# Optimization experiments

Measured on AMD Instinct MI355X. Metric: run time of the kernel, lower is better.

The kernel has to match this reference:

```python
import jax, jax.numpy as jnp
import numpy as np

B, C, H, W = 8, 1024, 32, 32   # batch, in_channels (cnn==vit), spatial
OUT = 2048                     # out_channels
NHEAD = 32                     # heads -> head_dim 64
EMBED_DIM = 1024               # used ONLY for the softmax scale (faithful to source)
LN_EPS = 1e-5


def setup_inputs() -> dict:
    key = jax.random.key(0)
    ks = jax.random.split(key, 8)
    f = lambda k, s: jax.random.normal(k, s, dtype=jnp.float32)
    return {
        "x_cnn": f(ks[0], (B, C, H, W)),
        "x_vit": f(ks[1], (B, C, H, W)),
        "Wq": f(ks[2], (OUT, C)) * 0.02, "bq": jnp.zeros((OUT,), jnp.float32),
        "Wk": f(ks[3], (OUT, C)) * 0.02, "bk": jnp.zeros((OUT,), jnp.float32),
        "Wv": f(ks[4], (OUT, C)) * 0.02, "bv": jnp.zeros((OUT,), jnp.float32),
        "w_mix": jnp.float32(0.5),
        "ln_g": jnp.ones((OUT,), jnp.float32), "ln_b": jnp.zeros((OUT,), jnp.float32),
        "Wfc": f(ks[5], (OUT, OUT)) * 0.02, "bfc": jnp.zeros((OUT,), jnp.float32),
    }


def _mha(Q, K, V):
    # Q,K,V: [b, n, OUT] -> multi-head attention, scale by sqrt(EMBED_DIM) as in source
    b, n, _ = Q.shape
    d = OUT // NHEAD
    Qh = Q.reshape(b, n, NHEAD, d)
    Kh = K.reshape(b, n, NHEAD, d)
    Vh = V.reshape(b, n, NHEAD, d)
    scores = jnp.einsum('bqhd,bkhd->bhqk', Qh, Kh) / jnp.sqrt(jnp.float32(EMBED_DIM))
    attn = jax.nn.softmax(scores, axis=-1)
    out = jnp.einsum('bhqk,bkhd->bqhd', attn, Vh)
    return out.reshape(b, n, OUT)


def reference(x_cnn, x_vit, Wq, bq, Wk, bk, Wv, bv, w_mix, ln_g, ln_b, Wfc, bfc):
    b, c, h, w = x_cnn.shape
    xc = x_cnn.reshape(b, c, h * w).transpose(0, 2, 1)   # [b, hw, c]
    xv = x_vit.reshape(b, c, h * w).transpose(0, 2, 1)
    # shared projections, two cross directions
    Q1 = xc @ Wq.T + bq; K1 = xv @ Wk.T + bk; V1 = xv @ Wv.T + bv
    Q2 = xv @ Wq.T + bq; K2 = xc @ Wk.T + bk; V2 = xc @ Wv.T + bv
    attended_vit = _mha(Q1, K1, V1)   # cnn queries attend vit
    attended_cnn = _mha(Q2, K2, V2)   # vit queries attend cnn
    r = attended_cnn * w_mix + attended_vit * (1.0 - w_mix)
    # LayerNorm over last dim (population variance, like torch)
    mu = jnp.mean(r, axis=-1, keepdims=True)
    var = jnp.var(r, axis=-1, keepdims=True)
    r = (r - mu) / jnp.sqrt(var + LN_EPS) * ln_g + ln_b
    r = r @ Wfc.T + bfc
    return r.transpose(0, 2, 1).reshape(b, OUT, h, w)
```

## Files before the change

### kernel.cpp

```cpp
#include <hip/hip_runtime.h>
#include <stdint.h>

typedef unsigned short u16;
typedef unsigned int u32;
typedef __attribute__((ext_vector_type(4))) float float4v;
typedef __attribute__((ext_vector_type(4))) unsigned int uint4v;
typedef __attribute__((ext_vector_type(4))) unsigned short u16x4;
typedef __attribute__((ext_vector_type(8))) short s16x8;
typedef __attribute__((ext_vector_type(4))) float f32x4;

__device__ __forceinline__ float bf2f(u16 h) {
    union { u32 u; float f; } v; v.u = ((u32)h) << 16; return v.f;
}
__device__ __forceinline__ u16 f2bf(float f) {
    union { float f; u32 u; } v; v.f = f;
    return (u16)((v.u + 0x8000u) >> 16);
}
__device__ __forceinline__ float exp2_fast(float x) {
    float r; asm("v_exp_f32 %0, %1" : "=v"(r) : "v"(x)); return r;
}

__device__ __forceinline__ bool detect_f32(const u16* lng) {
    return *(const u32*)lng == 0x3F800000u;
}

__device__ __forceinline__ float read_wmix(const void* wmix) {
    u32 word = *(const u32*)wmix;
    if ((word & 0xFFFFu) == 0u) {
        union { u32 u; float f; } v; v.u = word; return v.f;
    }
    return bf2f((u16)(word & 0xFFFFu));
}

__device__ __forceinline__ uint4v load8(const void* base, long long off, bool isF32) {
    if (isF32) {
        const float* p = (const float*)base + off;
        float4v f0 = *(const float4v*)p;
        float4v f1 = *(const float4v*)(p + 4);
        uint4v r; u16* h = (u16*)&r;
#pragma unroll
        for (int i = 0; i < 4; ++i) { h[i] = f2bf(f0[i]); h[4 + i] = f2bf(f1[i]); }
        return r;
    }
    return *(const uint4v*)((const u16*)base + off);
}
__device__ __forceinline__ float loadraw(const void* p, int idx, bool isF32) {
    return isF32 ? ((const float*)p)[idx] : bf2f(((const u16*)p)[idx]);
}

__global__ __launch_bounds__(256) void convert_w(
    const void* __restrict__ src, u16* __restrict__ dst, int n,
    const u16* __restrict__ lng)
{
    bool f32 = detect_f32(lng);
    long long i = ((long long)blockIdx.x * 256 + threadIdx.x) * 8;
    if (i >= n) return;
    uint4v v = load8(src, i, f32);
    *(uint4v*)(dst + i) = v;
}

__global__ __launch_bounds__(256) void transpose_k(
    const void* __restrict__ xc, const void* __restrict__ xv,
    u16* __restrict__ xt, const u16* __restrict__ lng)
{
    bool f32 = detect_f32(lng);
    int z = blockIdx.z;
    const void* xbase = (z < 8 ? xc : xv);
    long long soff = (long long)(z & 7) * 1024 * 1024;
    u16* outp = xt + (long long)z * 1024 * 1024;
    int c0 = blockIdx.x * 64, p0 = blockIdx.y * 64;
    __shared__ u16 t[64][72];
    int tid = threadIdx.x;
    int cl = tid >> 3, ch = tid & 7;
#pragma unroll
    for (int pass = 0; pass < 2; ++pass) {
        int c = cl + pass * 32;
        uint4v v = load8(xbase, soff + (long long)(c0 + c) * 1024 + p0 + ch * 8, f32);
        const u16* vv = (const u16*)&v;
#pragma unroll
        for (int i = 0; i < 8; ++i) t[ch * 8 + i][c] = vv[i];
    }
    __syncthreads();
#pragma unroll
    for (int pass = 0; pass < 2; ++pass) {
        int p = cl + pass * 32;
        uint4v v; u16* vv = (u16*)&v;
#pragma unroll
        for (int i = 0; i < 8; ++i) vv[i] = t[p][ch * 8 + i];
        *(uint4v*)(outp + (long long)(p0 + p) * 1024 + c0 + ch * 8) = v;
    }
}

__global__ __launch_bounds__(256) void transpose_v(
    const u16* __restrict__ V, u16* __restrict__ VT)
{
    int b = blockIdx.z, head = blockIdx.y, p0 = blockIdx.x * 64;
    const u16* src = V + (long long)b * 1024 * 2048 + head * 64;
    u16* dst = VT + (long long)(b * 32 + head) * 64 * 1024;
    __shared__ u16 t[64][72];
    int tid = threadIdx.x;
    int r = tid >> 3, ch = tid & 7;
#pragma unroll
    for (int pass = 0; pass < 2; ++pass) {
        int p = r + pass * 32;
        uint4v v = *(const uint4v*)(src + (long long)(p0 + p) * 2048 + ch * 8);
        const u16* vv = (const u16*)&v;
#pragma unroll
        for (int i = 0; i < 8; ++i) t[ch * 8 + i][p] = vv[i];
    }
    __syncthreads();
#pragma unroll
    for (int pass = 0; pass < 2; ++pass) {
        int d = r + pass * 32;
        uint4v v = *(const uint4v*)&t[d][ch * 8];
        *(uint4v*)(dst + (long long)d * 1024 + p0 + ch * 8) = v;
    }
}

__global__ __launch_bounds__(256) void gemm_mfma(
    const void* __restrict__ A, int lda, long long sA, int a_raw,
    const void* __restrict__ B, int ldb, long long sB, int b_raw,
    const void* __restrict__ bias,
    void* __restrict__ Cv, int ldc, long long sC, int c_f32,
    int K, int bias_on_m, const u16* __restrict__ lng)
{
    bool f32 = detect_f32(lng);
    bool aF = f32 && a_raw, bF = f32 && b_raw;
    int gx = gridDim.x, gy = gridDim.y, gz = gridDim.z;
    int flat = blockIdx.x + gx * (blockIdx.y + gy * blockIdx.z);
    int nwg = gx * gy * gz;
    int wsw = ((nwg & 7) == 0) ? ((flat & 7) * (nwg >> 3) + (flat >> 3)) : flat;
    int bxi = wsw % gx, rem = wsw / gx;
    int byi = rem % gy, z = rem / gy;

    long long aoff = (long long)z * sA, boff = (long long)z * sB;
    long long coff = (long long)z * sC;
    int m0 = bxi * 128, n0 = byi * 128;
    int tid = threadIdx.x;
    int lane = tid & 63, wave = tid >> 6;
    int lrow = lane & 15, lgrp = lane >> 4;
    int wm = (wave >> 1) * 64, wn = (wave & 1) * 64;

    __shared__ u16 As[128][72];
    __shared__ u16 Bs[128][72];

    f32x4 acc[4][4];
#pragma unroll
    for (int i = 0; i < 4; ++i)
#pragma unroll
        for (int j = 0; j < 4; ++j) acc[i][j] = (f32x4)0.f;

    int sr = tid >> 3;
    int kc = (tid & 7) * 8;

    long long arow[4], brow[4];
#pragma unroll
    for (int q = 0; q < 4; ++q) {
        arow[q] = aoff + (long long)(m0 + sr + q * 32) * lda;
        brow[q] = boff + (long long)(n0 + sr + q * 32) * ldb;
    }

    uint4v an[4], bn[4];
#pragma unroll
    for (int q = 0; q < 4; ++q) {
        an[q] = load8(A, arow[q] + kc, aF);
        bn[q] = load8(B, brow[q] + kc, bF);
    }

    for (int k0 = 0; k0 < K; k0 += 64) {
        uint4v ac[4], bc[4];
#pragma unroll
        for (int q = 0; q < 4; ++q) { ac[q] = an[q]; bc[q] = bn[q]; }
        __syncthreads();
#pragma unroll
        for (int q = 0; q < 4; ++q) {
            *(uint4v*)&As[sr + q * 32][kc] = ac[q];
            *(uint4v*)&Bs[sr + q * 32][kc] = bc[q];
        }
        __syncthreads();
        if (k0 + 64 < K) {
#pragma unroll
            for (int q = 0; q < 4; ++q) {
                an[q] = load8(A, arow[q] + k0 + 64 + kc, aF);
                bn[q] = load8(B, brow[q] + k0 + 64 + kc, bF);
            }
        }
#pragma unroll
        for (int kk = 0; kk < 2; ++kk) {
            s16x8 af[4], bfr[4];
#pragma unroll
            for (int i = 0; i < 4; ++i)
                af[i] = *(const s16x8*)&As[wm + i * 16 + lrow][kk * 32 + lgrp * 8];
#pragma unroll
            for (int j = 0; j < 4; ++j)
                bfr[j] = *(const s16x8*)&Bs[wn + j * 16 + lrow][kk * 32 + lgrp * 8];
#pragma unroll
            for (int i = 0; i < 4; ++i)
#pragma unroll
                for (int j = 0; j < 4; ++j)
                    acc[i][j] = __builtin_amdgcn_mfma_f32_16x16x32_bf16(
                        af[i], bfr[j], acc[i][j], 0, 0, 0);
        }
    }

    float bnj[4];
#pragma unroll
    for (int j = 0; j < 4; ++j)
        bnj[j] = bias_on_m ? 0.f : loadraw(bias, n0 + wn + j * 16 + lrow, f32);
#pragma unroll
    for (int i = 0; i < 4; ++i) {
#pragma unroll
        for (int e = 0; e < 4; ++e) {
            int mrow = m0 + wm + i * 16 + lgrp * 4 + e;
            float bm = bias_on_m ? loadraw(bias, mrow, f32) : 0.f;
#pragma unroll
            for (int j = 0; j < 4; ++j) {
                int ncol = n0 + wn + j * 16 + lrow;
                float val = acc[i][j][e] + (bias_on_m ? bm : bnj[j]);
                long long idx = coff + (long long)mrow * ldc + ncol;
                if (c_f32) ((float*)Cv)[idx] = val;
                else       ((u16*)Cv)[idx] = f2bf(val);
            }
        }
    }
}

__global__ __launch_bounds__(256) void attn_mfma(
    u16* __restrict__ Qb, const u16* __restrict__ Kb, const u16* __restrict__ VTb)
{
    const int ld = 2048;
    const float SCL = 0.0450985123f;
    int flat = blockIdx.x + 16 * (blockIdx.y + 32 * blockIdx.z);
    int w = (flat & 7) * 512 + (flat >> 3);
    int qt = w & 15, head = (w >> 4) & 31, bz = w >> 9;
    int q0 = qt * 64;
    long long base = (long long)bz * 1024 * ld + head * 64;
    u16* Q = Qb + base;
    const u16* K = Kb + base;
    const u16* VT = VTb + (long long)(bz * 32 + head) * 64 * 1024;

    int tid = threadIdx.x;
    int wave = tid >> 6, lane = tid & 63;
    int lrow = lane & 15, lgrp = lane >> 4;

    __shared__ u16 Kt[64][72];
    __shared__ u16 VTt[64][72];
    __shared__ u16 Pt[4][16][72];

    int qw = q0 + wave * 16;
    s16x8 qf0, qf1;
    {
        const u16* qp = Q + (long long)(qw + lrow) * ld + lgrp * 8;
        qf0 = *(const s16x8*)qp;
        qf1 = *(const s16x8*)(qp + 32);
    }

    f32x4 of[4];
#pragma unroll
    for (int dt = 0; dt < 4; ++dt) of[dt] = (f32x4)0.f;
    float mL = 0.f, l_run = 0.f;

    int skey = tid >> 2, sc4 = tid & 3;
    const u16* kptr = K + (long long)skey * ld + sc4 * 8;
    const u16* vptr = VT + (long long)skey * 1024 + sc4 * 16;
    uint4v ka0 = *(const uint4v*)kptr;
    uint4v ka1 = *(const uint4v*)(kptr + 32);
    uint4v va0 = *(const uint4v*)vptr;
    uint4v va1 = *(const uint4v*)(vptr + 8);

    for (int t = 0; t < 16; ++t) {
        *(uint4v*)&Kt[skey][sc4 * 8]       = ka0;
        *(uint4v*)&Kt[skey][sc4 * 8 + 32]  = ka1;
        *(uint4v*)&VTt[skey][sc4 * 16]     = va0;
        *(uint4v*)&VTt[skey][sc4 * 16 + 8] = va1;
        if (t < 15) {
            kptr += 64 * ld;
            vptr += 64;
            ka0 = *(const uint4v*)kptr;
            ka1 = *(const uint4v*)(kptr + 32);
            va0 = *(const uint4v*)vptr;
            va1 = *(const uint4v*)(vptr + 8);
        }
        __syncthreads();

        f32x4 sf[4];
#pragma unroll
        for (int f = 0; f < 4; ++f) {
            s16x8 kf0 = *(const s16x8*)&Kt[f * 16 + lrow][lgrp * 8];
            s16x8 kf1 = *(const s16x8*)&Kt[f * 16 + lrow][lgrp * 8 + 32];
            f32x4 a = (f32x4)0.f;
            a = __builtin_amdgcn_mfma_f32_16x16x32_bf16(kf0, qf0, a, 0, 0, 0);
            a = __builtin_amdgcn_mfma_f32_16x16x32_bf16(kf1, qf1, a, 0, 0, 0);
            sf[f] = a;
        }

        float mx = sf[0][0];
#pragma unroll
        for (int f = 0; f < 4; ++f)
#pragma unroll
            for (int i = 0; i < 4; ++i) mx = fmaxf(mx, sf[f][i]);
        mx = fmaxf(mx, __shfl_xor(mx, 16));
        mx = fmaxf(mx, __shfl_xor(mx, 32));
        if (__any(mx * SCL > mL + 8.f)) {
            float mLn = fmaxf(mL, mx * SCL);
            float sc = exp2_fast(mL - mLn);
            l_run *= sc;
#pragma unroll
            for (int dt = 0; dt < 4; ++dt)
#pragma unroll
                for (int i = 0; i < 4; ++i) of[dt][i] *= sc;
            mL = mLn;
        }

        float nmL = -mL, rs = 0.f;
#pragma unroll
        for (int f = 0; f < 4; ++f) {
            u16x4 pk;
#pragma unroll
            for (int i = 0; i < 4; ++i) {
                float pe = exp2_fast(fmaf(sf[f][i], SCL, nmL));
                rs += pe;
                pk[i] = f2bf(pe);
            }
            *(u16x4*)&Pt[wave][lrow][f * 16 + lgrp * 4] = pk;
        }
        rs += __shfl_xor(rs, 16);
        rs += __shfl_xor(rs, 32);
        l_run += rs;
        asm volatile("s_waitcnt lgkmcnt(0)" ::: "memory");
        __builtin_amdgcn_sched_barrier(0);

#pragma unroll
        for (int kk = 0; kk < 2; ++kk) {
            s16x8 pb = *(const s16x8*)&Pt[wave][lrow][kk * 32 + lgrp * 8];
#pragma unroll
            for (int dt = 0; dt < 4; ++dt) {
                s16x8 va = *(const s16x8*)&VTt[dt * 16 + lrow][kk * 32 + lgrp * 8];
                of[dt] = __builtin_amdgcn_mfma_f32_16x16x32_bf16(va, pb, of[dt], 0, 0, 0);
            }
        }
        __syncthreads();
    }

    float linv = 1.f / l_run;
#pragma unroll
    for (int dt = 0; dt < 4; ++dt) {
        u16x4 o;
#pragma unroll
        for (int i = 0; i < 4; ++i) o[i] = f2bf(of[dt][i] * linv);
        *(u16x4*)(Q + (long long)(qw + lrow) * ld + dt * 16 + lgrp * 4) = o;
    }
}

__global__ __launch_bounds__(256) void mix_ln_k(
    const u16* __restrict__ Avit, const u16* __restrict__ Acnn,
    const void* __restrict__ wmix,
    const void* __restrict__ g, const void* __restrict__ bta,
    u16* __restrict__ Y, const u16* __restrict__ lng)
{
    bool f32 = detect_f32(lng);
    long long row = blockIdx.x;
    const u16* a0 = Avit + row * 2048;
    const u16* a1 = Acnn + row * 2048;
    int tid = threadIdx.x, lane = tid & 63, wave = tid >> 6;
    float w = read_wmix(wmix);
    int o = tid * 8;
    uint4v x0 = *(const uint4v*)(a0 + o);
    uint4v x1 = *(const uint4v*)(a1 + o);
    const u16* p0 = (const u16*)&x0;
    const u16* p1 = (const u16*)&x1;
    float r[8], sum = 0.f, sq = 0.f;
#pragma unroll
    for (int e = 0; e < 8; ++e) {
        r[e] = w * bf2f(p1[e]) + (1.f - w) * bf2f(p0[e]);
        sum += r[e]; sq += r[e] * r[e];
    }
#pragma unroll
    for (int off = 1; off < 64; off <<= 1) {
        sum += __shfl_xor(sum, off);
        sq += __shfl_xor(sq, off);
    }
    __shared__ float red[8];
    if (lane == 0) { red[wave] = sum; red[4 + wave] = sq; }
    __syncthreads();
    sum = red[0] + red[1] + red[2] + red[3];
    sq = red[4] + red[5] + red[6] + red[7];
    float mu = sum * (1.f / 2048.f);
    float var = sq * (1.f / 2048.f) - mu * mu;
    float rstd = rsqrtf(var + 1e-5f);
    uint4v y; u16* py = (u16*)&y;
#pragma unroll
    for (int e = 0; e < 8; ++e)
        py[e] = f2bf((r[e] - mu) * rstd * loadraw(g, o + e, f32) + loadraw(bta, o + e, f32));
    *(uint4v*)(Y + row * 2048 + o) = y;
}

extern "C" void kernel_launch(void* const* d_in, const int* in_sizes, int n_in,
                              void* d_out, int out_size, void* d_ws, size_t ws_size,
                              hipStream_t stream)
{
    const void* x_cnn = d_in[0];
    const void* x_vit = d_in[1];
    const void* Wq = d_in[2];
    const void* bq = d_in[3];
    const void* Wk = d_in[4];
    const void* bk = d_in[5];
    const void* Wv = d_in[6];
    const void* bv = d_in[7];
    const void* wmix = d_in[8];
    const u16* ln_g = (const u16*)d_in[9];
    const void* ln_b = d_in[10];
    const void* Wfc = d_in[11];
    const void* bfc = d_in[12];

    u16* X   = (u16*)d_out;
    u16* VTb = (u16*)((char*)d_out + 33554432);
    char* ws = (char*)d_ws;
    u16* S0 = (u16*)ws;
    u16* S1 = (u16*)(ws + 1LL * 33554432);
    u16* S2 = (u16*)(ws + 2LL * 33554432);
    u16* S3 = (u16*)(ws + 3LL * 33554432);
    const long long SRC = 8LL * 1024 * 1024;

    const long long WS4 = 4LL * 33554432;
    bool tail = ws_size >= (size_t)(WS4 + 20971520LL);
    u16* WqB = (u16*)(ws + WS4);
    u16* WkB = WqB + 2097152;
    u16* WvB = WkB + 2097152;
    u16* WfB = WvB + 2097152;
    if (tail) {
        convert_w<<<1024, 256, 0, stream>>>(Wq, WqB, 2097152, ln_g);
        convert_w<<<1024, 256, 0, stream>>>(Wk, WkB, 2097152, ln_g);
        convert_w<<<1024, 256, 0, stream>>>(Wv, WvB, 2097152, ln_g);
        convert_w<<<2048, 256, 0, stream>>>(Wfc, WfB, 4194304, ln_g);
    }
    const void* pWq = tail ? (const void*)WqB : Wq;
    const void* pWk = tail ? (const void*)WkB : Wk;
    const void* pWv = tail ? (const void*)WvB : Wv;
    const void* pWf = tail ? (const void*)WfB : Wfc;
    int rawW = tail ? 0 : 1;

    transpose_k<<<dim3(16, 16, 16), 256, 0, stream>>>(x_cnn, x_vit, X, ln_g);

    dim3 pg(64, 16, 1);
    gemm_mfma<<<pg, 256, 0, stream>>>(X,       1024, 0LL, 0, pWq, 1024, 0LL, rawW, bq,
                                      S0, 2048, 0LL, 0, 1024, 0, ln_g);
    gemm_mfma<<<pg, 256, 0, stream>>>(X + SRC, 1024, 0LL, 0, pWk, 1024, 0LL, rawW, bk,
                                      S1, 2048, 0LL, 0, 1024, 0, ln_g);
    gemm_mfma<<<pg, 256, 0, stream>>>(X + SRC, 1024, 0LL, 0, pWv, 1024, 0LL, rawW, bv,
                                      S2, 2048, 0LL, 0, 1024, 0, ln_g);
    transpose_v<<<dim3(16, 32, 8), 256, 0, stream>>>(S2, VTb);
    attn_mfma<<<dim3(16, 32, 8), 256, 0, stream>>>(S0, S1, VTb);

    gemm_mfma<<<pg, 256, 0, stream>>>(X + SRC, 1024, 0LL, 0, pWq, 1024, 0LL, rawW, bq,
                                      S1, 2048, 0LL, 0, 1024, 0, ln_g);
    gemm_mfma<<<pg, 256, 0, stream>>>(X,       1024, 0LL, 0, pWk, 1024, 0LL, rawW, bk,
                                      S2, 2048, 0LL, 0, 1024, 0, ln_g);
    gemm_mfma<<<pg, 256, 0, stream>>>(X,       1024, 0LL, 0, pWv, 1024, 0LL, rawW, bv,
                                      S3, 2048, 0LL, 0, 1024, 0, ln_g);
    transpose_v<<<dim3(16, 32, 8), 256, 0, stream>>>(S3, VTb);
    attn_mfma<<<dim3(16, 32, 8), 256, 0, stream>>>(S1, S2, VTb);

    mix_ln_k<<<8192, 256, 0, stream>>>(S0, S1, wmix, ln_g, ln_b, S2, ln_g);

    gemm_mfma<<<dim3(16, 8, 8), 256, 0, stream>>>(pWf, 2048, 0LL, rawW, S2, 2048, 1024LL * 2048, 0, bfc,
                                                  d_out, 1024, 2048LL * 1024, 1, 2048, 1, ln_g);
}
```

Measured before the change: 924.1 us.

## Batch shared QKV projections over both sources and compute softmax row sums via MFMA

```diff
diff --git a/kernel.cpp b/kernel.cpp
--- a/kernel.cpp
+++ b/kernel.cpp
@@ -130,8 +130,8 @@
     int flat = blockIdx.x + gx * (blockIdx.y + gy * blockIdx.z);
     int nwg = gx * gy * gz;
     int wsw = ((nwg & 7) == 0) ? ((flat & 7) * (nwg >> 3) + (flat >> 3)) : flat;
-    int bxi = wsw % gx, rem = wsw / gx;
-    int byi = rem % gy, z = rem / gy;
+    int byi = wsw % gy, rem = wsw / gy;
+    int bxi = rem % gx, z = rem / gx;
 
     long long aoff = (long long)z * sA, boff = (long long)z * sB;
     long long coff = (long long)z * sC;
@@ -254,11 +254,15 @@
         qf0 = *(const s16x8*)qp;
         qf1 = *(const s16x8*)(qp + 32);
     }
+    s16x8 onesf;
+#pragma unroll
+    for (int e = 0; e < 8; ++e) ((u16*)&onesf)[e] = 0x3F80;
 
     f32x4 of[4];
 #pragma unroll
     for (int dt = 0; dt < 4; ++dt) of[dt] = (f32x4)0.f;
-    float mL = 0.f, l_run = 0.f;
+    f32x4 osum = (f32x4)0.f;
+    float mL = 0.f;
 
     int skey = tid >> 2, sc4 = tid & 3;
     const u16* kptr = K + (long long)skey * ld + sc4 * 8;
@@ -294,45 +298,47 @@
             sf[f] = a;
         }
 
-        float mx = sf[0][0];
-#pragma unroll
-        for (int f = 0; f < 4; ++f)
-#pragma unroll
-            for (int i = 0; i < 4; ++i) mx = fmaxf(mx, sf[f][i]);
+        float t0 = fmaxf(fmaxf(sf[0][0], sf[0][1]), sf[0][2]);
+        float t1 = fmaxf(fmaxf(sf[0][3], sf[1][0]), sf[1][1]);
+        float t2 = fmaxf(fmaxf(sf[1][2], sf[1][3]), sf[2][0]);
+        float t3 = fmaxf(fmaxf(sf[2][1], sf[2][2]), sf[2][3]);
+        float t4 = fmaxf(fmaxf(sf[3][0], sf[3][1]), sf[3][2]);
+        float u0 = fmaxf(fmaxf(t0, t1), t2);
+        float u1 = fmaxf(fmaxf(t3, t4), sf[3][3]);
+        float mx = fmaxf(u0, u1);
         mx = fmaxf(mx, __shfl_xor(mx, 16));
         mx = fmaxf(mx, __shfl_xor(mx, 32));
         if (__any(mx * SCL > mL + 8.f)) {
             float mLn = fmaxf(mL, mx * SCL);
             float sc = exp2_fast(mL - mLn);
-            l_run *= sc;
 #pragma unroll
             for (int dt = 0; dt < 4; ++dt)
 #pragma unroll
                 for (int i = 0; i < 4; ++i) of[dt][i] *= sc;
+#pragma unroll
+            for (int i = 0; i < 4; ++i) osum[i] *= sc;
             mL = mLn;
         }
 
-        float nmL = -mL, rs = 0.f;
+        float nmL = -mL;
 #pragma unroll
         for (int f = 0; f < 4; ++f) {
-            u16x4 pk;
-#pragma unroll
-            for (int i = 0; i < 4; ++i) {
-                float pe = exp2_fast(fmaf(sf[f][i], SCL, nmL));
-                rs += pe;
-                pk[i] = f2bf(pe);
-            }
-            *(u16x4*)&Pt[wave][lrow][f * 16 + lgrp * 4] = pk;
-        }
-        rs += __shfl_xor(rs, 16);
-        rs += __shfl_xor(rs, 32);
-        l_run += rs;
+            float p0 = exp2_fast(fmaf(sf[f][0], SCL, nmL));
+            float p1 = exp2_fast(fmaf(sf[f][1], SCL, nmL));
+            float p2 = exp2_fast(fmaf(sf[f][2], SCL, nmL));
+            float p3 = exp2_fast(fmaf(sf[f][3], SCL, nmL));
+            union { u32 w[2]; u16x4 v; } pu;
+            asm("v_cvt_pk_bf16_f32 %0, %1, %2" : "=v"(pu.w[0]) : "v"(p0), "v"(p1));
+            asm("v_cvt_pk_bf16_f32 %0, %1, %2" : "=v"(pu.w[1]) : "v"(p2), "v"(p3));
+            *(u16x4*)&Pt[wave][lrow][f * 16 + lgrp * 4] = pu.v;
+        }
         asm volatile("s_waitcnt lgkmcnt(0)" ::: "memory");
         __builtin_amdgcn_sched_barrier(0);
 
 #pragma unroll
         for (int kk = 0; kk < 2; ++kk) {
             s16x8 pb = *(const s16x8*)&Pt[wave][lrow][kk * 32 + lgrp * 8];
+            osum = __builtin_amdgcn_mfma_f32_16x16x32_bf16(onesf, pb, osum, 0, 0, 0);
 #pragma unroll
             for (int dt = 0; dt < 4; ++dt) {
                 s16x8 va = *(const s16x8*)&VTt[dt * 16 + lrow][kk * 32 + lgrp * 8];
@@ -342,7 +348,7 @@
         __syncthreads();
     }
 
-    float linv = 1.f / l_run;
+    float linv = 1.f / osum[0];
 #pragma unroll
     for (int dt = 0; dt < 4; ++dt) {
         u16x4 o;
@@ -416,15 +422,14 @@
     u16* X   = (u16*)d_out;
     u16* VTb = (u16*)((char*)d_out + 33554432);
     char* ws = (char*)d_ws;
-    u16* S0 = (u16*)ws;
-    u16* S1 = (u16*)(ws + 1LL * 33554432);
-    u16* S2 = (u16*)(ws + 2LL * 33554432);
-    u16* S3 = (u16*)(ws + 3LL * 33554432);
+    const long long SEG = 33554432LL;
     const long long SRC = 8LL * 1024 * 1024;
 
-    const long long WS4 = 4LL * 33554432;
-    bool tail = ws_size >= (size_t)(WS4 + 20971520LL);
-    u16* WqB = (u16*)(ws + WS4);
+    bool fused = ws_size >= (size_t)(6 * SEG + 20971520LL);
+    bool tail  = fused || ws_size >= (size_t)(4 * SEG + 20971520LL);
+    u16* S[6];
+    for (int i = 0; i < 6; ++i) S[i] = (u16*)(ws + i * SEG);
+    u16* WqB = (u16*)(ws + (fused ? 6 : 4) * SEG);
     u16* WkB = WqB + 2097152;
     u16* WvB = WkB + 2097152;
     u16* WfB = WvB + 2097152;
@@ -442,27 +447,40 @@
 
     transpose_k<<<dim3(16, 16, 16), 256, 0, stream>>>(x_cnn, x_vit, X, ln_g);
 
-    dim3 pg(64, 16, 1);
-    gemm_mfma<<<pg, 256, 0, stream>>>(X,       1024, 0LL, 0, pWq, 1024, 0LL, rawW, bq,
-                                      S0, 2048, 0LL, 0, 1024, 0, ln_g);
-    gemm_mfma<<<pg, 256, 0, stream>>>(X + SRC, 1024, 0LL, 0, pWk, 1024, 0LL, rawW, bk,
-                                      S1, 2048, 0LL, 0, 1024, 0, ln_g);
-    gemm_mfma<<<pg, 256, 0, stream>>>(X + SRC, 1024, 0LL, 0, pWv, 1024, 0LL, rawW, bv,
-                                      S2, 2048, 0LL, 0, 1024, 0, ln_g);
-    transpose_v<<<dim3(16, 32, 8), 256, 0, stream>>>(S2, VTb);
-    attn_mfma<<<dim3(16, 32, 8), 256, 0, stream>>>(S0, S1, VTb);
-
-    gemm_mfma<<<pg, 256, 0, stream>>>(X + SRC, 1024, 0LL, 0, pWq, 1024, 0LL, rawW, bq,
-                                      S1, 2048, 0LL, 0, 1024, 0, ln_g);
-    gemm_mfma<<<pg, 256, 0, stream>>>(X,       1024, 0LL, 0, pWk, 1024, 0LL, rawW, bk,
-                                      S2, 2048, 0LL, 0, 1024, 0, ln_g);
-    gemm_mfma<<<pg, 256, 0, stream>>>(X,       1024, 0LL, 0, pWv, 1024, 0LL, rawW, bv,
-                                      S3, 2048, 0LL, 0, 1024, 0, ln_g);
-    transpose_v<<<dim3(16, 32, 8), 256, 0, stream>>>(S3, VTb);
-    attn_mfma<<<dim3(16, 32, 8), 256, 0, stream>>>(S1, S2, VTb);
-
-    mix_ln_k<<<8192, 256, 0, stream>>>(S0, S1, wmix, ln_g, ln_b, S2, ln_g);
-
-    gemm_mfma<<<dim3(16, 8, 8), 256, 0, stream>>>(pWf, 2048, 0LL, rawW, S2, 2048, 1024LL * 2048, 0, bfc,
+    if (fused) {
+        dim3 fg(128, 16, 1);
+        gemm_mfma<<<fg, 256, 0, stream>>>(X, 1024, 0LL, 0, pWq, 1024, 0LL, rawW, bq,
+                                          S[0], 2048, 0LL, 0, 1024, 0, ln_g);
+        gemm_mfma<<<fg, 256, 0, stream>>>(X, 1024, 0LL, 0, pWk, 1024, 0LL, rawW, bk,
+                                          S[2], 2048, 0LL, 0, 1024, 0, ln_g);
+        gemm_mfma<<<fg, 256, 0, stream>>>(X, 1024, 0LL, 0, pWv, 1024, 0LL, rawW, bv,
+                                          S[4], 2048, 0LL, 0, 1024, 0, ln_g);
+        transpose_v<<<dim3(16, 32, 8), 256, 0, stream>>>(S[5], VTb);
+        attn_mfma<<<dim3(16, 32, 8), 256, 0, stream>>>(S[0], S[3], VTb);
+        transpose_v<<<dim3(16, 32, 8), 256, 0, stream>>>(S[4], VTb);
+        attn_mfma<<<dim3(16, 32, 8), 256, 0, stream>>>(S[1], S[2], VTb);
+        mix_ln_k<<<8192, 256, 0, stream>>>(S[0], S[1], wmix, ln_g, ln_b, S[2], ln_g);
+    } else {
+        dim3 pg(64, 16, 1);
+        gemm_mfma<<<pg, 256, 0, stream>>>(X,       1024, 0LL, 0, pWq, 1024, 0LL, rawW, bq,
+                                          S[0], 2048, 0LL, 0, 1024, 0, ln_g);
+        gemm_mfma<<<pg, 256, 0, stream>>>(X + SRC, 1024, 0LL, 0, pWk, 1024, 0LL, rawW, bk,
+                                          S[1], 2048, 0LL, 0, 1024, 0, ln_g);
+        gemm_mfma<<<pg, 256, 0, stream>>>(X + SRC, 1024, 0LL, 0, pWv, 1024, 0LL, rawW, bv,
+                                          S[2], 2048, 0LL, 0, 1024, 0, ln_g);
+        transpose_v<<<dim3(16, 32, 8), 256, 0, stream>>>(S[2], VTb);
+        attn_mfma<<<dim3(16, 32, 8), 256, 0, stream>>>(S[0], S[1], VTb);
+        gemm_mfma<<<pg, 256, 0, stream>>>(X + SRC, 1024, 0LL, 0, pWq, 1024, 0LL, rawW, bq,
+                                          S[1], 2048, 0LL, 0, 1024, 0, ln_g);
+        gemm_mfma<<<pg, 256, 0, stream>>>(X,       1024, 0LL, 0, pWk, 1024, 0LL, rawW, bk,
+                                          S[2], 2048, 0LL, 0, 1024, 0, ln_g);
+        gemm_mfma<<<pg, 256, 0, stream>>>(X,       1024, 0LL, 0, pWv, 1024, 0LL, rawW, bv,
+                                          S[3], 2048, 0LL, 0, 1024, 0, ln_g);
+        transpose_v<<<dim3(16, 32, 8), 256, 0, stream>>>(S[3], VTb);
+        attn_mfma<<<dim3(16, 32, 8), 256, 0, stream>>>(S[1], S[2], VTb);
+        mix_ln_k<<<8192, 256, 0, stream>>>(S[0], S[1], wmix, ln_g, ln_b, S[2], ln_g);
+    }
+
+    gemm_mfma<<<dim3(16, 8, 8), 256, 0, stream>>>(pWf, 2048, 0LL, rawW, S[2], 2048, 1024LL * 2048, 0, bfc,
                                                   d_out, 1024, 2048LL * 1024, 1, 2048, 1, ln_g);
 }
```

Measured after the change: 890.5 us. -3.6%, faster.
